# Kernel optimization log

Hardware: AMD Instinct MI355X
Metric: run time of the kernel (lower is better)

The kernel has to match this reference:

```python
import jax, jax.numpy as jnp
import numpy as np

B, C, H, W = 8, 192, 256, 256

def setup_inputs() -> dict:
    key = jax.random.key(0)
    k1, k2, k3, k4, k5 = jax.random.split(key, 5)
    x = jax.random.normal(k1, (B, C, H, W), dtype=jnp.float32)
    w1 = jax.random.normal(k2, (C, 1, 1, 1), dtype=jnp.float32) * 0.1
    w3 = jax.random.normal(k3, (C, 1, 3, 3), dtype=jnp.float32) * 0.1
    w5 = jax.random.normal(k4, (C, 1, 5, 5), dtype=jnp.float32) * 0.1
    alpha = jax.random.normal(k5, (4,), dtype=jnp.float32)
    return {"x": x, "w1": w1, "w3": w3, "w5": w5, "alpha": alpha}

def _dwconv(x, w, pad):
    # depthwise conv: feature_group_count == channels, kernel (C,1,k,k)
    return jax.lax.conv_general_dilated(
        x, w, window_strides=(1, 1), padding=[(pad, pad), (pad, pad)],
        dimension_numbers=("NCHW", "OIHW", "NCHW"),
        feature_group_count=x.shape[1])

def reference(x, w1, w3, w5, alpha):
    out1 = _dwconv(x, w1, 0)
    out3 = _dwconv(x, w3, 1)
    out5 = _dwconv(x, w5, 2)
    return alpha[0] * x + alpha[1] * out1 + alpha[2] * out3 + alpha[3] * out5
```

## Files before the change

### kernel.cpp

```cpp
#include <hip/hip_runtime.h>


constexpr int Bn = 8, Cn = 192, Hn = 256, Wn = 256;
constexpr int TR      = 32;
constexpr int LROWS   = TR + 4;
constexpr int LSTRIDE = 260;
constexpr int BANDS   = Hn / TR;

__global__ __launch_bounds__(256, 4)
void omnishift_kernel(const float* __restrict__ x,
                      const float* __restrict__ w1,
                      const float* __restrict__ w3,
                      const float* __restrict__ w5,
                      const float* __restrict__ alpha,
                      float* __restrict__ out)
{
    __shared__ float lds[LROWS * LSTRIDE];

    const int tid   = threadIdx.x;
    const int band  = blockIdx.x % BANDS;
    const int plane = blockIdx.x / BANDS;
    const int c     = plane % Cn;
    const int r0    = band * TR;

    const float a0 = alpha[0], a1 = alpha[1], a2 = alpha[2], a3 = alpha[3];
    float wf[5][5];
#pragma unroll
    for (int i = 0; i < 5; ++i)
#pragma unroll
        for (int j = 0; j < 5; ++j) {
            float v = a3 * w5[(c * 5 + i) * 5 + j];
            if (i >= 1 && i <= 3 && j >= 1 && j <= 3)
                v += a2 * w3[(c * 3 + (i - 1)) * 3 + (j - 1)];
            if (i == 2 && j == 2)
                v += a1 * w1[c] + a0;
            wf[i][j] = v;
        }

    const float* xp = x + (size_t)plane * (Hn * Wn);

    if (tid < LROWS * 4) {
        const int r   = tid >> 2;
        const int q   = tid & 3;
        const int col = (q < 2) ? q : (256 + q);
        lds[r * LSTRIDE + col] = 0.f;
    }

#pragma unroll
    for (int i = 0; i < 9; ++i) {
        const int fidx = tid + i * 256;
        const int row  = fidx >> 6;
        const int l    = fidx & 63;
        const int gr   = r0 - 2 + row;
        float4 v = make_float4(0.f, 0.f, 0.f, 0.f);
        if ((unsigned)gr < (unsigned)Hn)
            v = *reinterpret_cast<const float4*>(xp + gr * Wn + 4 * l);
        float* dst = &lds[row * LSTRIDE + 2 + 4 * l];
        *reinterpret_cast<float2*>(dst)     = make_float2(v.x, v.y);
        *reinterpret_cast<float2*>(dst + 2) = make_float2(v.z, v.w);
    }
    __syncthreads();

    const int ct     = tid & 63;
    const int rg     = tid >> 6;
    const int oc0    = 4 * ct;
    const int lrbase = rg * 8;

    float* outp = out + (size_t)plane * (Hn * Wn)
                      + (size_t)(r0 + rg * 8) * Wn + oc0;

    float win[5][8];
#pragma unroll
    for (int i = 0; i < 4; ++i) {
        const float* src = &lds[(lrbase + i) * LSTRIDE + oc0];
#pragma unroll
        for (int j = 0; j < 8; ++j) win[i][j] = src[j];
    }

#pragma unroll
    for (int k = 0; k < 8; ++k) {
        const float* src = &lds[(lrbase + 4 + k) * LSTRIDE + oc0];
#pragma unroll
        for (int j = 0; j < 8; ++j) win[4][j] = src[j];

        float o[4];
#pragma unroll
        for (int j = 0; j < 4; ++j) {
            float acc = 0.f;
#pragma unroll
            for (int i = 0; i < 5; ++i)
#pragma unroll
                for (int d = 0; d < 5; ++d)
                    acc += win[i][j + d] * wf[i][d];
            o[j] = acc;
        }
        *reinterpret_cast<float4*>(outp + (size_t)k * Wn) =
            make_float4(o[0], o[1], o[2], o[3]);

#pragma unroll
        for (int i = 0; i < 4; ++i)
#pragma unroll
            for (int j = 0; j < 8; ++j) win[i][j] = win[i + 1][j];
    }
}

extern "C" void kernel_launch(void* const* d_in, const int* in_sizes, int n_in,
                              void* d_out, int out_size, void* d_ws, size_t ws_size,
                              hipStream_t stream)
{
    const float* x     = (const float*)d_in[0];
    const float* w1    = (const float*)d_in[1];
    const float* w3    = (const float*)d_in[2];
    const float* w5    = (const float*)d_in[3];
    const float* alpha = (const float*)d_in[4];
    float* out = (float*)d_out;

    const int grid = Bn * Cn * BANDS;
    omnishift_kernel<<<grid, 256, 0, stream>>>(x, w1, w3, w5, alpha, out);
}
```

Measured before the change: 157.6 us.

## Process whole plane per block with ring-buffered LDS and prefetched rows

Each block now walks a full channel plane in 16-row phases instead of one 32-row band. It keeps a 36-slot circular LDS buffer and register-prefetches the next 16 rows from global memory while computing the current phase. This removes the 4-row halo reload per band and overlaps loads with compute. The trade-off is a grid of only 1536 blocks instead of 12288, a barrier per phase, and a manual vmcnt wait that may limit latency hiding.

```diff
diff --git a/kernel.cpp b/kernel.cpp
--- a/kernel.cpp
+++ b/kernel.cpp
@@ -1,11 +1,13 @@
 #include <hip/hip_runtime.h>
 
 
+typedef float f32x4 __attribute__((ext_vector_type(4)));
+
 constexpr int Bn = 8, Cn = 192, Hn = 256, Wn = 256;
-constexpr int TR      = 32;
-constexpr int LROWS   = TR + 4;
+constexpr int PH      = 16;
+constexpr int NPH     = Hn / PH;
+constexpr int SLOTS   = 36;
 constexpr int LSTRIDE = 260;
-constexpr int BANDS   = Hn / TR;
 
 __global__ __launch_bounds__(256, 4)
 void omnishift_kernel(const float* __restrict__ x,
@@ -15,13 +17,11 @@
                       const float* __restrict__ alpha,
                       float* __restrict__ out)
 {
-    __shared__ float lds[LROWS * LSTRIDE];
+    __shared__ float lds[SLOTS * LSTRIDE];
 
     const int tid   = threadIdx.x;
-    const int band  = blockIdx.x % BANDS;
-    const int plane = blockIdx.x / BANDS;
+    const int plane = blockIdx.x;
     const int c     = plane % Cn;
-    const int r0    = band * TR;
 
     const float a0 = alpha[0], a1 = alpha[1], a2 = alpha[2], a3 = alpha[3];
     float wf[5][5];
@@ -37,9 +37,10 @@
             wf[i][j] = v;
         }
 
-    const float* xp = x + (size_t)plane * (Hn * Wn);
+    const float* xp = x   + (size_t)plane * (Hn * Wn);
+    float*       op = out + (size_t)plane * (Hn * Wn);
 
-    if (tid < LROWS * 4) {
+    if (tid < SLOTS * 4) {
         const int r   = tid >> 2;
         const int q   = tid & 3;
         const int col = (q < 2) ? q : (256 + q);
@@ -47,60 +48,99 @@
     }
 
 #pragma unroll
-    for (int i = 0; i < 9; ++i) {
+    for (int i = 0; i < 5; ++i) {
         const int fidx = tid + i * 256;
         const int row  = fidx >> 6;
         const int l    = fidx & 63;
-        const int gr   = r0 - 2 + row;
+        const int gr   = row - 2;
         float4 v = make_float4(0.f, 0.f, 0.f, 0.f);
-        if ((unsigned)gr < (unsigned)Hn)
-            v = *reinterpret_cast<const float4*>(xp + gr * Wn + 4 * l);
+        if (gr >= 0) v = *reinterpret_cast<const float4*>(xp + gr * Wn + 4 * l);
         float* dst = &lds[row * LSTRIDE + 2 + 4 * l];
         *reinterpret_cast<float2*>(dst)     = make_float2(v.x, v.y);
         *reinterpret_cast<float2*>(dst + 2) = make_float2(v.z, v.w);
     }
     __syncthreads();
 
-    const int ct     = tid & 63;
-    const int rg     = tid >> 6;
-    const int oc0    = 4 * ct;
-    const int lrbase = rg * 8;
+    const int ct  = tid & 63;
+    const int rg  = tid >> 6;
+    const int oc0 = 4 * ct;
 
-    float* outp = out + (size_t)plane * (Hn * Wn)
-                      + (size_t)(r0 + rg * 8) * Wn + oc0;
+    int sbase = 0;
 
-    float win[5][8];
+#pragma unroll 1
+    for (int p = 0; p < NPH; ++p) {
+        float4 st[4];
+        if (p < NPH - 1) {
 #pragma unroll
-    for (int i = 0; i < 4; ++i) {
-        const float* src = &lds[(lrbase + i) * LSTRIDE + oc0];
+            for (int i = 0; i < 4; ++i) {
+                const int fidx = tid + i * 256;
+                const int row  = fidx >> 6;
+                const int l    = fidx & 63;
+                const int gr   = PH * p + 18 + row;
+                st[i] = make_float4(0.f, 0.f, 0.f, 0.f);
+                if (gr < Hn)
+                    st[i] = *reinterpret_cast<const float4*>(xp + gr * Wn + 4 * l);
+            }
+        }
+
+        float win[5][8];
 #pragma unroll
-        for (int j = 0; j < 8; ++j) win[i][j] = src[j];
-    }
+        for (int i = 0; i < 4; ++i) {
+            int slot = sbase + 4 * rg + i; if (slot >= SLOTS) slot -= SLOTS;
+            const float* src = &lds[slot * LSTRIDE + oc0];
+#pragma unroll
+            for (int j = 0; j < 8; ++j) win[i][j] = src[j];
+        }
+
+        f32x4 o[4];
+#pragma unroll
+        for (int k = 0; k < 4; ++k) {
+            int slot = sbase + 4 * rg + 4 + k; if (slot >= SLOTS) slot -= SLOTS;
+            const float* src = &lds[slot * LSTRIDE + oc0];
+#pragma unroll
+            for (int j = 0; j < 8; ++j) win[4][j] = src[j];
 
 #pragma unroll
-    for (int k = 0; k < 8; ++k) {
-        const float* src = &lds[(lrbase + 4 + k) * LSTRIDE + oc0];
+            for (int jj = 0; jj < 4; ++jj) {
+                float acc = 0.f;
 #pragma unroll
-        for (int j = 0; j < 8; ++j) win[4][j] = src[j];
+                for (int i = 0; i < 5; ++i)
+#pragma unroll
+                    for (int d = 0; d < 5; ++d)
+                        acc += win[i][jj + d] * wf[i][d];
+                o[k][jj] = acc;
+            }
+#pragma unroll
+            for (int i = 0; i < 4; ++i)
+#pragma unroll
+                for (int j = 0; j < 8; ++j) win[i][j] = win[i + 1][j];
+        }
 
-        float o[4];
+        if (p < NPH - 1) {
+            asm volatile("s_waitcnt vmcnt(0)" ::: "memory");
 #pragma unroll
-        for (int j = 0; j < 4; ++j) {
-            float acc = 0.f;
+            for (int i = 0; i < 4; ++i) {
+                const int fidx = tid + i * 256;
+                const int row  = fidx >> 6;
+                const int l    = fidx & 63;
+                int slot = sbase + 20 + row; if (slot >= SLOTS) slot -= SLOTS;
+                float* dst = &lds[slot * LSTRIDE + 2 + 4 * l];
+                *reinterpret_cast<float2*>(dst)     = make_float2(st[i].x, st[i].y);
+                *reinterpret_cast<float2*>(dst + 2) = make_float2(st[i].z, st[i].w);
+            }
+        }
+
+        float* outp = op + (size_t)(PH * p + 4 * rg) * Wn + oc0;
 #pragma unroll
-            for (int i = 0; i < 5; ++i)
-#pragma unroll
-                for (int d = 0; d < 5; ++d)
-                    acc += win[i][j + d] * wf[i][d];
-            o[j] = acc;
+        for (int k = 0; k < 4; ++k)
+            *reinterpret_cast<f32x4*>(outp + (size_t)k * Wn) = o[k];
+
+        if (p < NPH - 1) {
+            asm volatile("s_waitcnt lgkmcnt(0)" ::: "memory");
+            __builtin_amdgcn_s_barrier();
         }
-        *reinterpret_cast<float4*>(outp + (size_t)k * Wn) =
-            make_float4(o[0], o[1], o[2], o[3]);
 
-#pragma unroll
-        for (int i = 0; i < 4; ++i)
-#pragma unroll
-            for (int j = 0; j < 8; ++j) win[i][j] = win[i + 1][j];
+        sbase += PH; if (sbase >= SLOTS) sbase -= SLOTS;
     }
 }
 
@@ -115,6 +155,5 @@
     const float* alpha = (const float*)d_in[4];
     float* out = (float*)d_out;
 
-    const int grid = Bn * Cn * BANDS;
-    omnishift_kernel<<<grid, 256, 0, stream>>>(x, w1, w3, w5, alpha, out);
+    omnishift_kernel<<<Bn * Cn, 256, 0, stream>>>(x, w1, w3, w5, alpha, out);
 }
```

Measured after the change: 562.5 us. 3.57x slower.

## Replace LDS tiling with per-wave register streaming over 128-row bands

Applied to the files above, without the earlier changes.

Removes shared-memory staging and the block barrier; each wave now owns a 128-row half-plane and streams rows straight from global memory into a register sliding window. Halo columns come from extra float2 loads that overlap neighbouring lanes, edges are handled with clamped addresses and multiplicative masks, and the loads for the next four rows are prefetched into a rotating register buffer. This aims to hide load latency and drop LDS traffic, at the cost of redundant halo loads, higher register pressure, and far fewer blocks in the grid.

```diff
diff --git a/kernel.cpp b/kernel.cpp
--- a/kernel.cpp
+++ b/kernel.cpp
@@ -1,13 +1,15 @@
 #include <hip/hip_runtime.h>
 
 
+typedef float f32x4 __attribute__((ext_vector_type(4)));
+typedef float f32x2 __attribute__((ext_vector_type(2)));
+
 constexpr int Bn = 8, Cn = 192, Hn = 256, Wn = 256;
-constexpr int TR      = 32;
-constexpr int LROWS   = TR + 4;
-constexpr int LSTRIDE = 260;
-constexpr int BANDS   = Hn / TR;
+constexpr int HB = 128;
+constexpr int NWAVE = Bn * Cn * (Hn / HB);
+constexpr int NBLK  = NWAVE / 4;
 
-__global__ __launch_bounds__(256, 4)
+__global__ __launch_bounds__(256)
 void omnishift_kernel(const float* __restrict__ x,
                       const float* __restrict__ w1,
                       const float* __restrict__ w3,
@@ -15,13 +17,12 @@
                       const float* __restrict__ alpha,
                       float* __restrict__ out)
 {
-    __shared__ float lds[LROWS * LSTRIDE];
-
     const int tid   = threadIdx.x;
-    const int band  = blockIdx.x % BANDS;
-    const int plane = blockIdx.x / BANDS;
+    const int wid   = blockIdx.x * 4 + (tid >> 6);
+    const int band  = wid & 1;
+    const int plane = wid >> 1;
+    const int r0    = band * HB;
     const int c     = plane % Cn;
-    const int r0    = band * TR;
 
     const float a0 = alpha[0], a1 = alpha[1], a2 = alpha[2], a3 = alpha[3];
     float wf[5][5];
@@ -37,70 +38,77 @@
             wf[i][j] = v;
         }
 
-    const float* xp = x + (size_t)plane * (Hn * Wn);
+    const float* xp = x   + (size_t)plane * (Hn * Wn);
+    float*       op = out + (size_t)plane * (Hn * Wn);
 
-    if (tid < LROWS * 4) {
-        const int r   = tid >> 2;
-        const int q   = tid & 3;
-        const int col = (q < 2) ? q : (256 + q);
-        lds[r * LSTRIDE + col] = 0.f;
+    const int   ct    = tid & 63;
+    const int   c0    = 4 * ct;
+    const float maskL = (ct == 0)  ? 0.f : 1.f;
+    const float maskR = (ct == 63) ? 0.f : 1.f;
+    const int   colL  = (c0 - 2 < 0) ? 0 : c0 - 2;
+    const int   colR  = (c0 + 4 > Wn - 2) ? Wn - 2 : c0 + 4;
+
+    auto issue = [&](int gr, f32x4& C, f32x2& L, f32x2& R, float& m) {
+        int grc = gr < 0 ? 0 : (gr > Hn - 1 ? Hn - 1 : gr);
+        m = (gr == grc) ? 1.f : 0.f;
+        const float* rp = xp + (size_t)grc * Wn;
+        C = *reinterpret_cast<const f32x4*>(rp + c0);
+        L = *reinterpret_cast<const f32x2*>(rp + colL);
+        R = *reinterpret_cast<const f32x2*>(rp + colR);
+    };
+
+    float win[5][8];
+
+    {
+        f32x4 tC[4]; f32x2 tL[4], tR[4]; float tM[4];
+#pragma unroll
+        for (int i = 0; i < 4; ++i) issue(r0 - 2 + i, tC[i], tL[i], tR[i], tM[i]);
+#pragma unroll
+        for (int i = 0; i < 4; ++i) {
+            const float ml = maskL * tM[i], mc = tM[i], mr = maskR * tM[i];
+            win[i][0] = tL[i].x * ml;  win[i][1] = tL[i].y * ml;
+            win[i][2] = tC[i].x * mc;  win[i][3] = tC[i].y * mc;
+            win[i][4] = tC[i].z * mc;  win[i][5] = tC[i].w * mc;
+            win[i][6] = tR[i].x * mr;  win[i][7] = tR[i].y * mr;
+        }
     }
 
+    f32x4 sC[4]; f32x2 sL[4], sR[4]; float sM[4];
 #pragma unroll
-    for (int i = 0; i < 9; ++i) {
-        const int fidx = tid + i * 256;
-        const int row  = fidx >> 6;
-        const int l    = fidx & 63;
-        const int gr   = r0 - 2 + row;
-        float4 v = make_float4(0.f, 0.f, 0.f, 0.f);
-        if ((unsigned)gr < (unsigned)Hn)
-            v = *reinterpret_cast<const float4*>(xp + gr * Wn + 4 * l);
-        float* dst = &lds[row * LSTRIDE + 2 + 4 * l];
-        *reinterpret_cast<float2*>(dst)     = make_float2(v.x, v.y);
-        *reinterpret_cast<float2*>(dst + 2) = make_float2(v.z, v.w);
-    }
-    __syncthreads();
+    for (int i = 0; i < 4; ++i) issue(r0 + 2 + i, sC[i], sL[i], sR[i], sM[i]);
 
-    const int ct     = tid & 63;
-    const int rg     = tid >> 6;
-    const int oc0    = 4 * ct;
-    const int lrbase = rg * 8;
+#pragma unroll 1
+    for (int rb = 0; rb < HB; rb += 4) {
+#pragma unroll
+        for (int u = 0; u < 4; ++u) {
+            const int r = rb + u;
 
-    float* outp = out + (size_t)plane * (Hn * Wn)
-                      + (size_t)(r0 + rg * 8) * Wn + oc0;
+            const float ml = maskL * sM[u], mc = sM[u], mr = maskR * sM[u];
+            win[4][0] = sL[u].x * ml;  win[4][1] = sL[u].y * ml;
+            win[4][2] = sC[u].x * mc;  win[4][3] = sC[u].y * mc;
+            win[4][4] = sC[u].z * mc;  win[4][5] = sC[u].w * mc;
+            win[4][6] = sR[u].x * mr;  win[4][7] = sR[u].y * mr;
 
-    float win[5][8];
+            f32x4 o;
 #pragma unroll
-    for (int i = 0; i < 4; ++i) {
-        const float* src = &lds[(lrbase + i) * LSTRIDE + oc0];
+            for (int j = 0; j < 4; ++j) {
+                float acc = 0.f;
 #pragma unroll
-        for (int j = 0; j < 8; ++j) win[i][j] = src[j];
-    }
+                for (int i = 0; i < 5; ++i)
+#pragma unroll
+                    for (int d = 0; d < 5; ++d)
+                        acc += win[i][j + d] * wf[i][d];
+                o[j] = acc;
+            }
+            *reinterpret_cast<f32x4*>(op + (size_t)(r0 + r) * Wn + c0) = o;
+
+            issue(r0 + r + 6, sC[u], sL[u], sR[u], sM[u]);
 
 #pragma unroll
-    for (int k = 0; k < 8; ++k) {
-        const float* src = &lds[(lrbase + 4 + k) * LSTRIDE + oc0];
+            for (int i = 0; i < 4; ++i)
 #pragma unroll
-        for (int j = 0; j < 8; ++j) win[4][j] = src[j];
-
-        float o[4];
-#pragma unroll
-        for (int j = 0; j < 4; ++j) {
-            float acc = 0.f;
-#pragma unroll
-            for (int i = 0; i < 5; ++i)
-#pragma unroll
-                for (int d = 0; d < 5; ++d)
-                    acc += win[i][j + d] * wf[i][d];
-            o[j] = acc;
+                for (int j = 0; j < 8; ++j) win[i][j] = win[i + 1][j];
         }
-        *reinterpret_cast<float4*>(outp + (size_t)k * Wn) =
-            make_float4(o[0], o[1], o[2], o[3]);
-
-#pragma unroll
-        for (int i = 0; i < 4; ++i)
-#pragma unroll
-            for (int j = 0; j < 8; ++j) win[i][j] = win[i + 1][j];
     }
 }
 
@@ -115,6 +123,5 @@
     const float* alpha = (const float*)d_in[4];
     float* out = (float*)d_out;
 
-    const int grid = Bn * Cn * BANDS;
-    omnishift_kernel<<<grid, 256, 0, stream>>>(x, w1, w3, w5, alpha, out);
+    omnishift_kernel<<<NBLK, 256, 0, stream>>>(x, w1, w3, w5, alpha, out);
 }
```

After: 175.0 us. 1.11x slower.
